# Kernel tuning notes

Hardware: AMD Instinct MI355X
Metric: run time of the kernel (lower is better)

## Reference

```python
import jax, jax.numpy as jnp
import numpy as np
from jax import lax

K = 3
STRIDE = 1
PAD = 1


def _active_sites(mask):
    # mask: [B, Cm, H, W] int. A patch is 'active' if ANY element of the
    # unfolded (im2col) patch is nonzero -> max-pool of (mask != 0) over the
    # same kernel/stride/padding window.
    m = jnp.any(mask != 0, axis=1, keepdims=True).astype(jnp.float32)  # [B,1,H,W]
    pooled = lax.reduce_window(
        m, 0.0, lax.max,
        window_dimensions=(1, 1, K, K),
        window_strides=(1, 1, STRIDE, STRIDE),
        padding=((0, 0), (0, 0), (PAD, PAD), (PAD, PAD)))
    return pooled > 0  # [B,1,H_out,W_out] bool


def reference(x, mask, weight, bias):
    # Faithful math of MyConv: conv2d(x, weight) + bias at active patch sites
    # (patches whose mask window contains any nonzero), exact zeros elsewhere.
    # masked_scatter in the original preserves patch order, so this equals
    # active * (conv + bias).
    conv = lax.conv_general_dilated(
        x, weight,
        window_strides=(STRIDE, STRIDE),
        padding=((PAD, PAD), (PAD, PAD)),
        dimension_numbers=('NCHW', 'OIHW', 'NCHW'))  # [B,C_out,H_out,W_out]
    active = _active_sites(mask)
    out = (conv + bias[None, :, None, None]) * active.astype(conv.dtype)
    return out


def setup_inputs() -> dict:
    key = jax.random.key(0)
    k1, k2, k3, k4 = jax.random.split(key, 4)
    B, C_in, C_out, H, W = 8, 128, 128, 128, 128
    x = jax.random.normal(k1, (B, C_in, H, W), dtype=jnp.float32)
    mask = jax.random.randint(k2, (B, 1, H, W), 0, 2, dtype=jnp.int32)
    fan_in = C_in * K * K
    bound = 1.0 / np.sqrt(fan_in)
    weight = jax.random.uniform(k3, (C_out, C_in, K, K), minval=-bound, maxval=bound, dtype=jnp.float32)
    bias = jax.random.uniform(k4, (C_out,), minval=-bound, maxval=bound, dtype=jnp.float32)
    return {"x": x, "mask": mask, "weight": weight, "bias": bias}
```

## Files before the change

### kernel.cpp

```cpp
#include <hip/hip_runtime.h>


typedef __bf16 bf16x8 __attribute__((ext_vector_type(8)));
typedef unsigned short u16x8 __attribute__((ext_vector_type(8)));
typedef float f32x4 __attribute__((ext_vector_type(4)));

__device__ __forceinline__ unsigned short f2bf(float f) {
    unsigned int u = __float_as_uint(f);
    u += 0x7fffu + ((u >> 16) & 1u);
    return (unsigned short)(u >> 16);
}

__global__ void setup_all(const float* __restrict__ x, const float* __restrict__ wgt,
                          unsigned short* __restrict__ xp, unsigned short* __restrict__ wpp) {
    __shared__ float Lf[32 * 132];
    const int t   = threadIdx.x;
    const int bid = blockIdx.x;

    if (bid >= 4160) {
        const int e    = (bid - 4160) * 256 + t;
        const int j    = e & 31;
        const int m    = (e >> 5) & 127;
        const int r    = e >> 12;
        const int kw   = r - (r / 3) * 3;
        const int cbkh = r / 3;
        const int cb   = cbkh & 3;
        const int kh   = cbkh >> 2;
        wpp[e] = f2bf(wgt[((m * 128 + cb * 32 + j) * 3 + kh) * 3 + kw]);
        return;
    }

    const int hh2 = bid % 130;
    const int cb  = (bid / 130) & 3;
    const int b   = bid / 520;
    u16x8* slab = (u16x8*)(xp + (size_t)(((b * 4 + cb) * 130 + hh2)) * 4160);
    const u16x8 z = {0, 0, 0, 0, 0, 0, 0, 0};

    if (hh2 == 0 || hh2 == 129) {
        for (int k = t; k < 520; k += 256) slab[k] = z;
        return;
    }
    const int h = hh2 - 1;

    #pragma unroll
    for (int u = 0; u < 4; ++u) {
        const int f  = t + 256 * u;
        const int ci = f >> 5;
        const int w4 = f & 31;
        const float4 v = *(const float4*)(x + (((b * 128 + cb * 32 + ci) * 128 + h) << 7) + (w4 << 2));
        *(float4*)&Lf[ci * 132 + (w4 << 2)] = v;
    }
    __syncthreads();

    for (int k = t; k < 520; k += 256) {
        const int r = k >> 2;
        const int c = k & 3;
        u16x8 o;
        if (r == 0 || r == 129) {
            o = z;
        } else {
            const int w   = r - 1;
            const int ci0 = (c ^ ((r + (r >> 2)) & 3)) << 3;
            #pragma unroll
            for (int s = 0; s < 8; ++s) o[s] = f2bf(Lf[(ci0 + s) * 132 + w]);
        }
        slab[k] = o;
    }
}

__device__ __forceinline__ void stage_slabs(const unsigned char* gx, unsigned char* ls, int t) {
    const int g    = t >> 6;
    const int lane = t & 63;
    #pragma unroll
    for (int u = 0; u < 8; ++u)
        __builtin_amdgcn_global_load_lds(
            (const __attribute__((address_space(1))) unsigned int*)(gx + u * 2048 + g * 1024 + lane * 16),
            (__attribute__((address_space(3))) unsigned int*)(ls + u * 2048 + g * 1024),
            16, 0, 0);
    if (t < 16)
        __builtin_amdgcn_global_load_lds(
            (const __attribute__((address_space(1))) unsigned int*)(gx + 16384 + t * 16),
            (__attribute__((address_space(3))) unsigned int*)(ls + 16384),
            16, 0, 0);
}

__global__ __launch_bounds__(128, 2)
void myconv5(const unsigned short* __restrict__ xp,
             const int* __restrict__ mask,
             const unsigned short* __restrict__ wp,
             const float* __restrict__ bias,
             float* __restrict__ out)
{
    __shared__ __align__(16) unsigned char Xs[2][16640];
    __shared__ float act[256];

    const int t     = threadIdx.x;
    const int b     = blockIdx.x >> 7;
    const int mhalf = (blockIdx.x >> 6) & 1;
    const int h0    = (blockIdx.x & 63) << 1;

    const int lane = t & 63;
    const int l16  = lane & 15;
    const int q    = lane >> 4;
    const int g    = t >> 6;

    const unsigned char* xpB = (const unsigned char*)xp;

    stage_slabs(xpB + (size_t)((b * 4 + 0) * 130 + h0 + 0) * 8320, &Xs[0][0], t);

    #pragma unroll
    for (int gg = 0; gg < 2; ++gg) {
        const int h = h0 + gg;
        int any = 0;
        #pragma unroll
        for (int kh = 0; kh < 3; ++kh) {
            int hh = h + kh - 1;
            if ((unsigned)hh < 128u) {
                const int* mrow = mask + (b * 128 + hh) * 128;
                #pragma unroll
                for (int kw = 0; kw < 3; ++kw) {
                    int ww = t + kw - 1;
                    if ((unsigned)ww < 128u) any |= mrow[ww];
                }
            }
        }
        act[gg * 128 + t] = any ? 1.0f : 0.0f;
    }

    int bb[3];
    #pragma unroll
    for (int kw = 0; kw < 3; ++kw) {
        const int rr   = l16 + kw;
        const int slot = q ^ ((rr + (rr >> 2)) & 3);
        bb[kw] = g * 8320 + rr * 64 + (slot << 4);
    }

    const unsigned char* agl = (const unsigned char*)wp + (mhalf * 64 + l16) * 64 + q * 16;

    f32x4 acc[4][8];
    const f32x4 fzero = {0.f, 0.f, 0.f, 0.f};
    #pragma unroll
    for (int i = 0; i < 4; ++i)
        #pragma unroll
        for (int j = 0; j < 8; ++j)
            acc[i][j] = fzero;

    __syncthreads();

    for (int r = 0; r < 12; ++r) {
        if (r < 11) {
            const int rn = r + 1;
            stage_slabs(xpB + (size_t)((b * 4 + (rn & 3)) * 130 + h0 + (rn >> 2)) * 8320,
                        &Xs[(rn & 1)][0], t);
        }

        const unsigned char* ar = agl + r * 24576;
        const unsigned char* xb = &Xs[r & 1][0];
        #pragma unroll
        for (int kw = 0; kw < 3; ++kw) {
            bf16x8 af[4];
            #pragma unroll
            for (int i = 0; i < 4; ++i)
                af[i] = *(const bf16x8*)(ar + kw * 8192 + i * 1024);
            bf16x8 bfr[8];
            #pragma unroll
            for (int j = 0; j < 8; ++j)
                bfr[j] = *(const bf16x8*)(xb + bb[kw] + j * 1024);
            #pragma unroll
            for (int i = 0; i < 4; ++i)
                #pragma unroll
                for (int j = 0; j < 8; ++j)
                    acc[i][j] = __builtin_amdgcn_mfma_f32_16x16x32_bf16(af[i], bfr[j], acc[i][j], 0, 0, 0);
        }

        __syncthreads();
    }

    #pragma unroll
    for (int i = 0; i < 4; ++i) {
        const int m0 = mhalf * 64 + (i << 4) + (q << 2);
        const f32x4 bv = *(const f32x4*)(bias + m0);
        #pragma unroll
        for (int j = 0; j < 8; ++j) {
            const int w = (j << 4) + l16;
            const float a = act[(g << 7) + w];
            float* base = out + (((b << 7) + m0) << 14) + ((h0 + g) << 7) + w;
            #pragma unroll
            for (int rg = 0; rg < 4; ++rg)
                base[rg << 14] = (acc[i][j][rg] + bv[rg]) * a;
        }
    }
}

#define LDAF 40
__global__ __launch_bounds__(256, 2)
void myconv_fb(const float* __restrict__ x,
               const int* __restrict__ mask,
               const float* __restrict__ wgt,
               const float* __restrict__ bias,
               float* __restrict__ out)
{
    __shared__ unsigned short As[128 * LDAF];
    __shared__ unsigned short Bs[128 * LDAF];
    __shared__ float act[128];

    const int t   = threadIdx.x;
    const int blk = blockIdx.x;
    const int b   = blk >> 7;
    const int h   = blk & 127;

    if (t < 128) {
        int any = 0;
        #pragma unroll
        for (int kh = 0; kh < 3; ++kh) {
            int hh = h + kh - 1;
            if ((unsigned)hh < 128u) {
                const int* mrow = mask + (b * 128 + hh) * 128;
                #pragma unroll
                for (int kw = 0; kw < 3; ++kw) {
                    int ww = t + kw - 1;
                    if ((unsigned)ww < 128u) any |= mrow[ww];
                }
            }
        }
        act[t] = any ? 1.0f : 0.0f;
    }

    const int lane = t & 63;
    const int l16  = lane & 15;
    const int half = lane >> 4;
    const int wv   = t >> 6;
    const int wm   = (wv >> 1) << 6;
    const int wn   = (wv & 1) << 6;

    f32x4 acc[4][4];
    const f32x4 fzero = {0.f, 0.f, 0.f, 0.f};
    #pragma unroll
    for (int i = 0; i < 4; ++i)
        #pragma unroll
        for (int j = 0; j < 4; ++j)
            acc[i][j] = fzero;

    const int am  = t >> 3;
    const int ac4 = (t & 7) << 2;
    const int n     = t & 127;
    const int khalf = __builtin_amdgcn_readfirstlane(t >> 7);
    const int xb    = b << 21;

    for (int kt = 0; kt < 36; ++kt) {
        __syncthreads();
        #pragma unroll
        for (int jj = 0; jj < 4; ++jj) {
            const int m = am + (jj << 5);
            const float4 v = *(const float4*)(wgt + m * 1152 + kt * 32 + ac4);
            unsigned short* dst = &As[m * LDAF + ac4];
            dst[0] = f2bf(v.x); dst[1] = f2bf(v.y); dst[2] = f2bf(v.z); dst[3] = f2bf(v.w);
        }
        u16x8 bv0, bv1;
        #pragma unroll
        for (int s = 0; s < 16; ++s) {
            const int k  = kt * 32 + khalf * 16 + s;
            const int ci = (k * 7282) >> 16;
            const int r  = k - ci * 9;
            const int kh = (r >= 3) + (r >= 6);
            const int kw = r - kh * 3;
            const int hh = h + kh - 1;
            float v = 0.f;
            if ((unsigned)hh < 128u) {
                const int ww = n + kw - 1;
                if ((unsigned)ww < 128u)
                    v = x[xb + (ci << 14) + (hh << 7) + ww];
            }
            if (s < 8) bv0[s] = f2bf(v); else bv1[s - 8] = f2bf(v);
        }
        *(u16x8*)&Bs[n * LDAF + khalf * 16]     = bv0;
        *(u16x8*)&Bs[n * LDAF + khalf * 16 + 8] = bv1;

        __syncthreads();

        bf16x8 af[4], bfr[4];
        #pragma unroll
        for (int i = 0; i < 4; ++i)
            af[i] = *(const bf16x8*)&As[(wm + (i << 4) + l16) * LDAF + (half << 3)];
        #pragma unroll
        for (int j = 0; j < 4; ++j)
            bfr[j] = *(const bf16x8*)&Bs[(wn + (j << 4) + l16) * LDAF + (half << 3)];
        #pragma unroll
        for (int i = 0; i < 4; ++i)
            #pragma unroll
            for (int j = 0; j < 4; ++j)
                acc[i][j] = __builtin_amdgcn_mfma_f32_16x16x32_bf16(af[i], bfr[j], acc[i][j], 0, 0, 0);
    }

    #pragma unroll
    for (int i = 0; i < 4; ++i) {
        #pragma unroll
        for (int j = 0; j < 4; ++j) {
            const int ncol = wn + (j << 4) + l16;
            const float a  = act[ncol];
            #pragma unroll
            for (int rg = 0; rg < 4; ++rg) {
                const int m = wm + (i << 4) + (half << 2) + rg;
                out[(((b << 7) + m) << 14) + (h << 7) + ncol] =
                    (acc[i][j][rg] + bias[m]) * a;
            }
        }
    }
}

extern "C" void kernel_launch(void* const* d_in, const int* in_sizes, int n_in,
                              void* d_out, int out_size, void* d_ws, size_t ws_size,
                              hipStream_t stream) {
    const float* x    = (const float*)d_in[0];
    const int*   mask = (const int*)d_in[1];
    const float* wgt  = (const float*)d_in[2];
    const float* bias = (const float*)d_in[3];
    float* out        = (float*)d_out;

    const size_t XP_ELEMS = 4160ull * 4160;
    const size_t WP_ELEMS = 36ull * 128 * 32;
    const size_t need = (XP_ELEMS + WP_ELEMS) * 2;

    if (ws_size >= need) {
        unsigned short* xpw = (unsigned short*)d_ws;
        unsigned short* wpw = xpw + XP_ELEMS;
        setup_all<<<dim3(4736), dim3(256), 0, stream>>>(x, wgt, xpw, wpw);
        myconv5<<<dim3(1024), dim3(128), 0, stream>>>(xpw, mask, wpw, bias, out);
    } else {
        myconv_fb<<<dim3(1024), dim3(256), 0, stream>>>(x, mask, wgt, bias, out);
    }
}
```

Before: 151.5 us.

## Split conv work per block into one row, all channels, four waves

Reorganizes the conv kernel so each 256-thread block handles one output row for all 128 output channels, with waves split across channel halves and column halves. The block stages a single input slab per round instead of two, accumulators shrink to 16 per wave, and launch bounds allow more resident waves. The aim is higher occupancy and no duplicated input staging across channel-half blocks. In exchange, weight fragments are fetched by twice as many waves, and each wave does fewer MFMAs per load.

```diff
diff --git a/kernel.cpp b/kernel.cpp
--- a/kernel.cpp
+++ b/kernel.cpp
@@ -68,49 +68,48 @@
     }
 }
 
-__device__ __forceinline__ void stage_slabs(const unsigned char* gx, unsigned char* ls, int t) {
+__device__ __forceinline__ void stage_slab(const unsigned char* gx, unsigned char* ls, int t) {
     const int g    = t >> 6;
     const int lane = t & 63;
     #pragma unroll
-    for (int u = 0; u < 8; ++u)
+    for (int u = 0; u < 2; ++u)
         __builtin_amdgcn_global_load_lds(
-            (const __attribute__((address_space(1))) unsigned int*)(gx + u * 2048 + g * 1024 + lane * 16),
-            (__attribute__((address_space(3))) unsigned int*)(ls + u * 2048 + g * 1024),
+            (const __attribute__((address_space(1))) unsigned int*)(gx + u * 4096 + g * 1024 + lane * 16),
+            (__attribute__((address_space(3))) unsigned int*)(ls + u * 4096 + g * 1024),
             16, 0, 0);
-    if (t < 16)
+    if (t < 8)
         __builtin_amdgcn_global_load_lds(
-            (const __attribute__((address_space(1))) unsigned int*)(gx + 16384 + t * 16),
-            (__attribute__((address_space(3))) unsigned int*)(ls + 16384),
+            (const __attribute__((address_space(1))) unsigned int*)(gx + 8192 + t * 16),
+            (__attribute__((address_space(3))) unsigned int*)(ls + 8192),
             16, 0, 0);
 }
 
-__global__ __launch_bounds__(128, 2)
-void myconv5(const unsigned short* __restrict__ xp,
+__global__ __launch_bounds__(256, 4)
+void myconv6(const unsigned short* __restrict__ xp,
              const int* __restrict__ mask,
              const unsigned short* __restrict__ wp,
              const float* __restrict__ bias,
              float* __restrict__ out)
 {
-    __shared__ __align__(16) unsigned char Xs[2][16640];
-    __shared__ float act[256];
-
-    const int t     = threadIdx.x;
-    const int b     = blockIdx.x >> 7;
-    const int mhalf = (blockIdx.x >> 6) & 1;
-    const int h0    = (blockIdx.x & 63) << 1;
+    __shared__ __align__(16) unsigned char Xs[2][8320];
+    __shared__ float act[128];
+
+    const int t = threadIdx.x;
+    const int b = blockIdx.x >> 7;
+    const int h = blockIdx.x & 127;
 
     const int lane = t & 63;
     const int l16  = lane & 15;
     const int q    = lane >> 4;
     const int g    = t >> 6;
+    const int mh   = g & 1;
+    const int nh   = g >> 1;
 
     const unsigned char* xpB = (const unsigned char*)xp;
 
-    stage_slabs(xpB + (size_t)((b * 4 + 0) * 130 + h0 + 0) * 8320, &Xs[0][0], t);
-
-    #pragma unroll
-    for (int gg = 0; gg < 2; ++gg) {
-        const int h = h0 + gg;
+    stage_slab(xpB + (size_t)((b * 4 + 0) * 130 + h + 0) * 8320, &Xs[0][0], t);
+
+    if (t < 128) {
         int any = 0;
         #pragma unroll
         for (int kh = 0; kh < 3; ++kh) {
@@ -124,7 +123,7 @@
                 }
             }
         }
-        act[gg * 128 + t] = any ? 1.0f : 0.0f;
+        act[t] = any ? 1.0f : 0.0f;
     }
 
     int bb[3];
@@ -132,17 +131,17 @@
     for (int kw = 0; kw < 3; ++kw) {
         const int rr   = l16 + kw;
         const int slot = q ^ ((rr + (rr >> 2)) & 3);
-        bb[kw] = g * 8320 + rr * 64 + (slot << 4);
-    }
-
-    const unsigned char* agl = (const unsigned char*)wp + (mhalf * 64 + l16) * 64 + q * 16;
-
-    f32x4 acc[4][8];
+        bb[kw] = nh * 4096 + rr * 64 + (slot << 4);
+    }
+
+    const unsigned char* agl = (const unsigned char*)wp + (mh * 64 + l16) * 64 + q * 16;
+
+    f32x4 acc[4][4];
     const f32x4 fzero = {0.f, 0.f, 0.f, 0.f};
     #pragma unroll
     for (int i = 0; i < 4; ++i)
         #pragma unroll
-        for (int j = 0; j < 8; ++j)
+        for (int j = 0; j < 4; ++j)
             acc[i][j] = fzero;
 
     __syncthreads();
@@ -150,8 +149,8 @@
     for (int r = 0; r < 12; ++r) {
         if (r < 11) {
             const int rn = r + 1;
-            stage_slabs(xpB + (size_t)((b * 4 + (rn & 3)) * 130 + h0 + (rn >> 2)) * 8320,
-                        &Xs[(rn & 1)][0], t);
+            stage_slab(xpB + (size_t)((b * 4 + (rn & 3)) * 130 + h + (rn >> 2)) * 8320,
+                       &Xs[(rn & 1)][0], t);
         }
 
         const unsigned char* ar = agl + r * 24576;
@@ -162,14 +161,14 @@
             #pragma unroll
             for (int i = 0; i < 4; ++i)
                 af[i] = *(const bf16x8*)(ar + kw * 8192 + i * 1024);
-            bf16x8 bfr[8];
-            #pragma unroll
-            for (int j = 0; j < 8; ++j)
+            bf16x8 bfr[4];
+            #pragma unroll
+            for (int j = 0; j < 4; ++j)
                 bfr[j] = *(const bf16x8*)(xb + bb[kw] + j * 1024);
             #pragma unroll
             for (int i = 0; i < 4; ++i)
                 #pragma unroll
-                for (int j = 0; j < 8; ++j)
+                for (int j = 0; j < 4; ++j)
                     acc[i][j] = __builtin_amdgcn_mfma_f32_16x16x32_bf16(af[i], bfr[j], acc[i][j], 0, 0, 0);
         }
 
@@ -178,13 +177,13 @@
 
     #pragma unroll
     for (int i = 0; i < 4; ++i) {
-        const int m0 = mhalf * 64 + (i << 4) + (q << 2);
+        const int m0 = mh * 64 + (i << 4) + (q << 2);
         const f32x4 bv = *(const f32x4*)(bias + m0);
         #pragma unroll
-        for (int j = 0; j < 8; ++j) {
-            const int w = (j << 4) + l16;
-            const float a = act[(g << 7) + w];
-            float* base = out + (((b << 7) + m0) << 14) + ((h0 + g) << 7) + w;
+        for (int j = 0; j < 4; ++j) {
+            const int w = nh * 64 + (j << 4) + l16;
+            const float a = act[w];
+            float* base = out + (((b << 7) + m0) << 14) + (h << 7) + w;
             #pragma unroll
             for (int rg = 0; rg < 4; ++rg)
                 base[rg << 14] = (acc[i][j][rg] + bv[rg]) * a;
@@ -325,7 +324,7 @@
         unsigned short* xpw = (unsigned short*)d_ws;
         unsigned short* wpw = xpw + XP_ELEMS;
         setup_all<<<dim3(4736), dim3(256), 0, stream>>>(x, wgt, xpw, wpw);
-        myconv5<<<dim3(1024), dim3(128), 0, stream>>>(xpw, mask, wpw, bias, out);
+        myconv6<<<dim3(1024), dim3(256), 0, stream>>>(xpw, mask, wpw, bias, out);
     } else {
         myconv_fb<<<dim3(1024), dim3(256), 0, stream>>>(x, mask, wgt, bias, out);
     }
```

After: 158.8 us. 1.05x slower.
